# Performance work log

Measured on AMD Instinct MI355X. Metric: run time of the kernel, lower is better.

Reference implementation:

```python
import jax, jax.numpy as jnp
import numpy as np

N = 524288
D = 256
NUM_SEGMENTS = 8192


def setup_inputs() -> dict:
    key = jax.random.key(0)
    k = jax.random.split(key, 6)
    s = 1.0 / np.sqrt(D)
    s2 = 1.0 / np.sqrt(2 * D)
    return {
        "x": jax.random.normal(k[0], (N, D), dtype=jnp.float32),
        "batch_index": jnp.sort(jax.random.randint(k[1], (N,), 0, NUM_SEGMENTS, dtype=jnp.int32)),
        "W1": jax.random.uniform(k[2], (D, D), jnp.float32, -s, s),
        "b1": jax.random.uniform(k[3], (D,), jnp.float32, -s, s),
        "Wp": jax.random.uniform(k[4], (D, 2 * D), jnp.float32, -s2, s2),
        "bp": jax.random.uniform(k[5], (D,), jnp.float32, -s2, s2),
    }


def reference(x, batch_index, W1, b1, Wp, bp):
    # prepool linear: [N, D]
    h = x @ W1.T + b1
    # scatter-mean over groups
    seg_sum = jax.ops.segment_sum(h, batch_index, num_segments=NUM_SEGMENTS)
    counts = jax.ops.segment_sum(jnp.ones((h.shape[0],), h.dtype), batch_index, num_segments=NUM_SEGMENTS)
    xmean = seg_sum / jnp.maximum(counts, 1.0)[:, None]
    # scatter-max over groups (empty segments -> 0, matching torch_scatter default fill; they are never gathered)
    xmax = jax.ops.segment_max(h, batch_index, num_segments=NUM_SEGMENTS)
    xmax = jnp.where(jnp.isfinite(xmax), xmax, jnp.zeros_like(xmax))
    # meanmax concat -> proj -> gather back to entities
    xpool = jnp.concatenate([xmean, xmax], axis=1)  # [B, 2D]
    out = xpool @ Wp.T + bp  # [B, D]
    return out[batch_index]  # [N, D]
```

## Files before the change

### kernel.cpp

```cpp
#include <hip/hip_runtime.h>

#define NROWS 524288
#define DIM 256
#define NSEG 8192
#define SPB 8
#define SEGS3 8

typedef __attribute__((ext_vector_type(8))) short bf16x8;
typedef __attribute__((ext_vector_type(4))) float f32x4;

__device__ __forceinline__ short f2bf(float f) {
  union { float f; unsigned u; } a; a.f = f;
  unsigned r = a.u + 0x7fffu + ((a.u >> 16) & 1u);
  return (short)(r >> 16);
}

__global__ void seg_start_kernel(const int* __restrict__ bi, int* __restrict__ ss) {
  int s = blockIdx.x * blockDim.x + threadIdx.x;
  if (s > NSEG) return;
  int lo = 0, hi = NROWS;
  while (lo < hi) { int mid = (lo + hi) >> 1; if (bi[mid] < s) lo = mid + 1; else hi = mid; }
  ss[s] = lo;
}

__global__ __launch_bounds__(256, 2) void gemm_pool_kernel(
    const float* __restrict__ x, const float* __restrict__ W1,
    const float* __restrict__ b1, const int* __restrict__ ss,
    float* __restrict__ xpool) {
  __shared__ short x_lds[2][16 * 264];

  const int tid  = threadIdx.x;
  const int wave = tid >> 6, lane = tid & 63;
  const int quad = lane >> 4, l16 = lane & 15;

  const int s0i = blockIdx.x * SPB;
  const int r0 = ss[s0i];
  const int r1 = ss[s0i + SPB];
  if (r0 >= r1) return;

  bf16x8 bfr[4][8];
  #pragma unroll
  for (int tt = 0; tt < 4; ++tt) {
    const int col = wave * 64 + tt * 16 + l16;
    #pragma unroll
    for (int ks = 0; ks < 8; ++ks) {
      const float* p = W1 + (size_t)col * DIM + ks * 32 + quad * 8;
      f32x4 w0 = *(const f32x4*)p;
      f32x4 w1 = *(const f32x4*)(p + 4);
      bf16x8 f;
      f[0]=f2bf(w0[0]); f[1]=f2bf(w0[1]); f[2]=f2bf(w0[2]); f[3]=f2bf(w0[3]);
      f[4]=f2bf(w1[0]); f[5]=f2bf(w1[1]); f[6]=f2bf(w1[2]); f[7]=f2bf(w1[3]);
      bfr[tt][ks] = f;
    }
  }
  const float b1f = b1[wave * 64 + quad * 16 + l16];

  const int srow = tid >> 4;
  const int scol = (tid & 15) * 16;

  int idx = 0;
  int seg_lo = r0;
  int seg_hi = ss[s0i + 1];
  while (seg_hi == seg_lo) { ++idx; seg_lo = seg_hi; seg_hi = ss[s0i + idx + 1]; }

  float ssum[4] = {0.f, 0.f, 0.f, 0.f};
  float smax[4] = {-3.0e38f, -3.0e38f, -3.0e38f, -3.0e38f};
  f32x4 acc[4];

  auto issue_loads = [&](int prow, f32x4& v0, f32x4& v1, f32x4& v2, f32x4& v3) -> bool {
    bool pf = (prow < r1);
    if (pf) {
      const f32x4* xp = (const f32x4*)(x + (size_t)prow * DIM + scol);
      v0 = __builtin_nontemporal_load(xp);
      v1 = __builtin_nontemporal_load(xp + 1);
      v2 = __builtin_nontemporal_load(xp + 2);
      v3 = __builtin_nontemporal_load(xp + 3);
    }
    return pf;
  };
  auto stage_write = [&](int buf, const f32x4& v0, const f32x4& v1,
                         const f32x4& v2, const f32x4& v3) {
    bf16x8 a0, a1;
    a0[0]=f2bf(v0[0]); a0[1]=f2bf(v0[1]); a0[2]=f2bf(v0[2]); a0[3]=f2bf(v0[3]);
    a0[4]=f2bf(v1[0]); a0[5]=f2bf(v1[1]); a0[6]=f2bf(v1[2]); a0[7]=f2bf(v1[3]);
    a1[0]=f2bf(v2[0]); a1[1]=f2bf(v2[1]); a1[2]=f2bf(v2[2]); a1[3]=f2bf(v2[3]);
    a1[4]=f2bf(v3[0]); a1[5]=f2bf(v3[1]); a1[6]=f2bf(v3[2]); a1[7]=f2bf(v3[3]);
    short* dst = &x_lds[buf][srow * 264 + scol];
    *(bf16x8*)dst = a0;
    *(bf16x8*)(dst + 8) = a1;
  };
  auto compute_chunk = [&](int c) {
    const int base = r0 + c * 16;
    int nr = r1 - base; if (nr > 16) nr = 16;
    const short* xb = x_lds[c & 1];
    acc[0] = (f32x4){0.f,0.f,0.f,0.f}; acc[1] = (f32x4){0.f,0.f,0.f,0.f};
    acc[2] = (f32x4){0.f,0.f,0.f,0.f}; acc[3] = (f32x4){0.f,0.f,0.f,0.f};
    #pragma unroll
    for (int ks = 0; ks < 8; ++ks) {
      bf16x8 a = *(const bf16x8*)&xb[l16 * 264 + ks * 32 + quad * 8];
      acc[0] = __builtin_amdgcn_mfma_f32_16x16x32_bf16(a, bfr[0][ks], acc[0], 0, 0, 0);
      acc[1] = __builtin_amdgcn_mfma_f32_16x16x32_bf16(a, bfr[1][ks], acc[1], 0, 0, 0);
      acc[2] = __builtin_amdgcn_mfma_f32_16x16x32_bf16(a, bfr[2][ks], acc[2], 0, 0, 0);
      acc[3] = __builtin_amdgcn_mfma_f32_16x16x32_bf16(a, bfr[3][ks], acc[3], 0, 0, 0);
    }
    int r = 0;
    while (r < nr) {
      int e = seg_hi - base; if (e > nr) e = nr;
      if (r == 0 && e == 16) {
        #pragma unroll
        for (int tt = 0; tt < 4; ++tt) {
          ssum[tt] += (acc[tt][0] + acc[tt][1]) + (acc[tt][2] + acc[tt][3]);
          smax[tt] = fmaxf(smax[tt], fmaxf(fmaxf(acc[tt][0], acc[tt][1]),
                                           fmaxf(acc[tt][2], acc[tt][3])));
        }
      } else {
        #pragma unroll
        for (int tt = 0; tt < 4; ++tt) {
          #pragma unroll
          for (int j = 0; j < 4; ++j) {
            const int row = (quad << 2) + j;
            const bool in = (row >= r) && (row < e);
            ssum[tt] += in ? acc[tt][j] : 0.f;
            smax[tt] = in ? fmaxf(smax[tt], acc[tt][j]) : smax[tt];
          }
        }
      }
      if (base + e == seg_hi) {
        float c0 = ssum[0], c1 = ssum[1], c2 = ssum[2], c3 = ssum[3];
        c0 += __shfl_xor(c0, 16); c0 += __shfl_xor(c0, 32);
        c1 += __shfl_xor(c1, 16); c1 += __shfl_xor(c1, 32);
        c2 += __shfl_xor(c2, 16); c2 += __shfl_xor(c2, 32);
        c3 += __shfl_xor(c3, 16); c3 += __shfl_xor(c3, 32);
        float m0 = smax[0], m1 = smax[1], m2 = smax[2], m3 = smax[3];
        m0 = fmaxf(m0, __shfl_xor(m0, 16)); m0 = fmaxf(m0, __shfl_xor(m0, 32));
        m1 = fmaxf(m1, __shfl_xor(m1, 16)); m1 = fmaxf(m1, __shfl_xor(m1, 32));
        m2 = fmaxf(m2, __shfl_xor(m2, 16)); m2 = fmaxf(m2, __shfl_xor(m2, 32));
        m3 = fmaxf(m3, __shfl_xor(m3, 16)); m3 = fmaxf(m3, __shfl_xor(m3, 32));
        const float fs = (quad & 2) ? ((quad & 1) ? c3 : c2) : ((quad & 1) ? c1 : c0);
        const float fm = (quad & 2) ? ((quad & 1) ? m3 : m2) : ((quad & 1) ? m1 : m0);
        const float inv = 1.f / (float)(seg_hi - seg_lo);
        const int col = wave * 64 + quad * 16 + l16;
        xpool[(size_t)(s0i + idx) * 512 + col]       = fs * inv + b1f;
        xpool[(size_t)(s0i + idx) * 512 + 256 + col] = fm + b1f;
        ssum[0]=0.f; ssum[1]=0.f; ssum[2]=0.f; ssum[3]=0.f;
        smax[0]=-3.0e38f; smax[1]=-3.0e38f; smax[2]=-3.0e38f; smax[3]=-3.0e38f;
        if (base + e < r1) {
          do { ++idx; seg_lo = seg_hi; seg_hi = ss[s0i + idx + 1]; } while (seg_hi == seg_lo);
        }
      }
      r = e;
    }
  };

  const int nch = (r1 - r0 + 15) >> 4;

  f32x4 a0v, a1v, a2v, a3v, b0v, b1v_, b2v, b3v;
  bool pfa = false, pfb = false;
  {
    bool p0 = issue_loads(r0 + srow, b0v, b1v_, b2v, b3v);
    if (p0) stage_write(0, b0v, b1v_, b2v, b3v);
  }
  pfa = issue_loads(r0 + 16 + srow, a0v, a1v, a2v, a3v);
  __syncthreads();

  for (int c = 0; c < nch; c += 2) {
    pfb = issue_loads(r0 + (c + 2) * 16 + srow, b0v, b1v_, b2v, b3v);
    compute_chunk(c);
    if (pfa) stage_write((c + 1) & 1, a0v, a1v, a2v, a3v);
    __syncthreads();
    if (c + 1 >= nch) break;
    pfa = issue_loads(r0 + (c + 3) * 16 + srow, a0v, a1v, a2v, a3v);
    compute_chunk(c + 1);
    if (pfb) stage_write(c & 1, b0v, b1v_, b2v, b3v);
    __syncthreads();
  }
}

__global__ __launch_bounds__(256) void proj_kernel(
    const float* __restrict__ xpool, const float* __restrict__ Wp,
    const float* __restrict__ bp, float* __restrict__ out_pool) {
  __shared__ float xp_lds[SEGS3 * 512];
  const int tid = threadIdx.x;
  const size_t s0 = (size_t)blockIdx.x * SEGS3;
  for (int i = tid; i < SEGS3 * 128; i += 256)
    *(f32x4*)&xp_lds[i * 4] = *(const f32x4*)&xpool[s0 * 512 + (size_t)i * 4];
  __syncthreads();
  float acc[SEGS3];
  #pragma unroll
  for (int s = 0; s < SEGS3; ++s) acc[s] = 0.f;
  for (int k0 = 0; k0 < 512; k0 += 4) {
    f32x4 wp = *(const f32x4*)&Wp[(size_t)tid * 512 + k0];
    #pragma unroll
    for (int s = 0; s < SEGS3; ++s) {
      f32x4 xv = *(const f32x4*)&xp_lds[s * 512 + k0];
      acc[s] += xv[0]*wp[0] + xv[1]*wp[1] + xv[2]*wp[2] + xv[3]*wp[3];
    }
  }
  const float b = bp[tid];
  #pragma unroll
  for (int s = 0; s < SEGS3; ++s)
    out_pool[(s0 + s) * 256 + tid] = acc[s] + b;
}

__global__ __launch_bounds__(256) void gather_kernel(
    const int* __restrict__ ss, const float* __restrict__ out_pool,
    float* __restrict__ out) {
  const int s = blockIdx.x;
  const int lo = ss[s], hi = ss[s + 1];
  if (lo >= hi) return;
  const int tid = threadIdx.x;
  const int rofs = tid >> 6;
  const int c4 = tid & 63;
  const f32x4 v = *(const f32x4*)&out_pool[(size_t)s * 256 + (size_t)c4 * 4];
  for (int n = lo + rofs; n < hi; n += 4)
    __builtin_nontemporal_store(v, (f32x4*)&out[(size_t)n * 256 + (size_t)c4 * 4]);
}

extern "C" void kernel_launch(void* const* d_in, const int* in_sizes, int n_in,
                              void* d_out, int out_size, void* d_ws, size_t ws_size,
                              hipStream_t stream) {
  const float* x  = (const float*)d_in[0];
  const int*   bi = (const int*)d_in[1];
  const float* W1 = (const float*)d_in[2];
  const float* b1 = (const float*)d_in[3];
  const float* Wp = (const float*)d_in[4];
  const float* bp = (const float*)d_in[5];
  float* out = (float*)d_out;

  char* ws = (char*)d_ws;
  int*   ss       = (int*)ws;
  float* xpool    = (float*)(ws + 64 * 1024);
  float* out_pool = (float*)(ws + 64 * 1024 + (size_t)NSEG * 512 * 4);

  seg_start_kernel<<<(NSEG + 256) / 256, 256, 0, stream>>>(bi, ss);
  gemm_pool_kernel<<<NSEG / SPB, 256, 0, stream>>>(x, W1, b1, ss, xpool);
  proj_kernel<<<NSEG / SEGS3, 256, 0, stream>>>(xpool, Wp, bp, out_pool);
  gather_kernel<<<NSEG, 256, 0, stream>>>(ss, out_pool, out);
}
```

Baseline: 1.061 ms.

## Fuse projection with gather and use lightweight LDS-only barriers in GEMM pool

Merges the projection and gather kernels into one, so each thread computes one output column for 8 segments and writes it directly to all rows of each segment. This removes the out_pool round trip and one kernel launch. The projection now reads xpool straight from global memory instead of staging it in LDS, and uses vectorized 8-wide accumulation. The gemm_pool kernel swaps __syncthreads for a barrier that waits only on LDS counters, letting outstanding global prefetches stay in flight across the barrier. The cost is that the fused kernel writes scalar floats per row rather than 16-byte vectors, and its write phase is serialized within each block.

```diff
diff --git a/kernel.cpp b/kernel.cpp
--- a/kernel.cpp
+++ b/kernel.cpp
@@ -13,6 +13,13 @@
   union { float f; unsigned u; } a; a.f = f;
   unsigned r = a.u + 0x7fffu + ((a.u >> 16) & 1u);
   return (short)(r >> 16);
+}
+
+__device__ __forceinline__ void lds_barrier() {
+  asm volatile("s_waitcnt lgkmcnt(0)" ::: "memory");
+  __builtin_amdgcn_sched_barrier(0);
+  __builtin_amdgcn_s_barrier();
+  __builtin_amdgcn_sched_barrier(0);
 }
 
 __global__ void seg_start_kernel(const int* __restrict__ bi, int* __restrict__ ss) {
@@ -161,59 +168,51 @@
     if (p0) stage_write(0, b0v, b1v_, b2v, b3v);
   }
   pfa = issue_loads(r0 + 16 + srow, a0v, a1v, a2v, a3v);
-  __syncthreads();
+  lds_barrier();
 
   for (int c = 0; c < nch; c += 2) {
     pfb = issue_loads(r0 + (c + 2) * 16 + srow, b0v, b1v_, b2v, b3v);
     compute_chunk(c);
     if (pfa) stage_write((c + 1) & 1, a0v, a1v, a2v, a3v);
-    __syncthreads();
+    lds_barrier();
     if (c + 1 >= nch) break;
     pfa = issue_loads(r0 + (c + 3) * 16 + srow, a0v, a1v, a2v, a3v);
     compute_chunk(c + 1);
     if (pfb) stage_write(c & 1, b0v, b1v_, b2v, b3v);
-    __syncthreads();
-  }
-}
-
-__global__ __launch_bounds__(256) void proj_kernel(
+    lds_barrier();
+  }
+}
+
+__global__ __launch_bounds__(256) void proj_gather_kernel(
     const float* __restrict__ xpool, const float* __restrict__ Wp,
-    const float* __restrict__ bp, float* __restrict__ out_pool) {
-  __shared__ float xp_lds[SEGS3 * 512];
+    const float* __restrict__ bp, const int* __restrict__ ss,
+    float* __restrict__ out) {
   const int tid = threadIdx.x;
-  const size_t s0 = (size_t)blockIdx.x * SEGS3;
-  for (int i = tid; i < SEGS3 * 128; i += 256)
-    *(f32x4*)&xp_lds[i * 4] = *(const f32x4*)&xpool[s0 * 512 + (size_t)i * 4];
-  __syncthreads();
-  float acc[SEGS3];
+  const int s0 = blockIdx.x * SEGS3;
+
+  f32x4 acc4[SEGS3];
   #pragma unroll
-  for (int s = 0; s < SEGS3; ++s) acc[s] = 0.f;
-  for (int k0 = 0; k0 < 512; k0 += 4) {
-    f32x4 wp = *(const f32x4*)&Wp[(size_t)tid * 512 + k0];
+  for (int s = 0; s < SEGS3; ++s) acc4[s] = (f32x4){0.f, 0.f, 0.f, 0.f};
+
+  const float* wrow = Wp + (size_t)tid * 512;
+  for (int k0 = 0; k0 < 512; k0 += 8) {
+    f32x4 wp0 = *(const f32x4*)(wrow + k0);
+    f32x4 wp1 = *(const f32x4*)(wrow + k0 + 4);
     #pragma unroll
     for (int s = 0; s < SEGS3; ++s) {
-      f32x4 xv = *(const f32x4*)&xp_lds[s * 512 + k0];
-      acc[s] += xv[0]*wp[0] + xv[1]*wp[1] + xv[2]*wp[2] + xv[3]*wp[3];
+      f32x4 xv0 = *(const f32x4*)&xpool[(size_t)(s0 + s) * 512 + k0];
+      f32x4 xv1 = *(const f32x4*)&xpool[(size_t)(s0 + s) * 512 + k0 + 4];
+      acc4[s] += xv0 * wp0 + xv1 * wp1;
     }
   }
   const float b = bp[tid];
   #pragma unroll
-  for (int s = 0; s < SEGS3; ++s)
-    out_pool[(s0 + s) * 256 + tid] = acc[s] + b;
-}
-
-__global__ __launch_bounds__(256) void gather_kernel(
-    const int* __restrict__ ss, const float* __restrict__ out_pool,
-    float* __restrict__ out) {
-  const int s = blockIdx.x;
-  const int lo = ss[s], hi = ss[s + 1];
-  if (lo >= hi) return;
-  const int tid = threadIdx.x;
-  const int rofs = tid >> 6;
-  const int c4 = tid & 63;
-  const f32x4 v = *(const f32x4*)&out_pool[(size_t)s * 256 + (size_t)c4 * 4];
-  for (int n = lo + rofs; n < hi; n += 4)
-    __builtin_nontemporal_store(v, (f32x4*)&out[(size_t)n * 256 + (size_t)c4 * 4]);
+  for (int s = 0; s < SEGS3; ++s) {
+    const float v = (acc4[s][0] + acc4[s][1]) + (acc4[s][2] + acc4[s][3]) + b;
+    const int lo = ss[s0 + s], hi = ss[s0 + s + 1];
+    for (int n = lo; n < hi; ++n)
+      __builtin_nontemporal_store(v, &out[(size_t)n * 256 + tid]);
+  }
 }
 
 extern "C" void kernel_launch(void* const* d_in, const int* in_sizes, int n_in,
@@ -228,12 +227,10 @@
   float* out = (float*)d_out;
 
   char* ws = (char*)d_ws;
-  int*   ss       = (int*)ws;
-  float* xpool    = (float*)(ws + 64 * 1024);
-  float* out_pool = (float*)(ws + 64 * 1024 + (size_t)NSEG * 512 * 4);
+  int*   ss    = (int*)ws;
+  float* xpool = (float*)(ws + 64 * 1024);
 
   seg_start_kernel<<<(NSEG + 256) / 256, 256, 0, stream>>>(bi, ss);
   gemm_pool_kernel<<<NSEG / SPB, 256, 0, stream>>>(x, W1, b1, ss, xpool);
-  proj_kernel<<<NSEG / SEGS3, 256, 0, stream>>>(xpool, Wp, bp, out_pool);
-  gather_kernel<<<NSEG, 256, 0, stream>>>(ss, out_pool, out);
-}
+  proj_gather_kernel<<<NSEG / SEGS3, 256, 0, stream>>>(xpool, Wp, bp, ss, out);
+}
```

Result: faster. 1.037 ms (-2.2%).
